# Performance work log

Measured on AMD Instinct MI355X. Metric: run time of the kernel, lower is better.

The kernel has to match this reference:

```python
import jax, jax.numpy as jnp
import numpy as np

N_NODES = 100000
N_EDGES = 1000000
DIM = 64
N_GRAPHS = 256
OUT_DIM = 10
BN_EPS = 1e-5


def setup_inputs() -> dict:
    key = jax.random.key(0)
    ks = jax.random.split(key, 12)
    s = 0.1  # weight init scale
    x = jax.random.normal(ks[0], (N_NODES, DIM), jnp.float32)
    edge_index = jax.random.randint(ks[1], (2, N_EDGES), 0, N_NODES, dtype=jnp.int32)
    batch = jnp.sort(jax.random.randint(ks[2], (N_NODES,), 0, N_GRAPHS, dtype=jnp.int32))
    w1 = jax.random.normal(ks[3], (3, DIM, DIM), jnp.float32) * s
    b1 = jax.random.normal(ks[4], (3, DIM), jnp.float32) * s
    w2 = jax.random.normal(ks[5], (3, DIM, DIM), jnp.float32) * s
    b2 = jax.random.normal(ks[6], (3, DIM), jnp.float32) * s
    gamma = jax.random.uniform(ks[7], (3, DIM), jnp.float32, 0.5, 1.5)
    beta = jax.random.normal(ks[8], (3, DIM), jnp.float32) * s
    eps_g = jnp.zeros((3,), jnp.float32)  # GIN train_eps, init 0
    lin_w = jax.random.normal(ks[9], (DIM, OUT_DIM), jnp.float32) * s
    lin_b = jax.random.normal(ks[10], (OUT_DIM,), jnp.float32) * s
    return dict(x=x, edge_index=edge_index, batch=batch, w1=w1, b1=b1,
                w2=w2, b2=b2, gamma=gamma, beta=beta, eps_g=eps_g,
                lin_w=lin_w, lin_b=lin_b)


def _gin_layer(x, src, dst, w1, b1, w2, b2, gamma, beta, eps):
    # scatter-add neighbor aggregation: agg[i] = sum_{(j->i) in E} x[j]
    agg = jax.ops.segment_sum(x[src], dst, num_segments=N_NODES)
    h = (1.0 + eps) * x + agg
    h = jax.nn.relu(h @ w1 + b1)
    h = jax.nn.relu(h @ w2 + b2)
    # BatchNorm1d, training-mode batch statistics (biased variance)
    mean = jnp.mean(h, axis=0)
    var = jnp.mean((h - mean) ** 2, axis=0)
    h = (h - mean) * jax.lax.rsqrt(var + BN_EPS) * gamma + beta
    return jax.nn.relu(h)  # outer F.relu(conv(...))


def reference(x, edge_index, batch, w1, b1, w2, b2, gamma, beta, eps_g, lin_w, lin_b):
    src, dst = edge_index[0], edge_index[1]
    for i in range(3):
        x = _gin_layer(x, src, dst, w1[i], b1[i], w2[i], b2[i],
                       gamma[i], beta[i], eps_g[i])
    # global mean pool over graphs
    sums = jax.ops.segment_sum(x, batch, num_segments=N_GRAPHS)
    counts = jax.ops.segment_sum(jnp.ones((x.shape[0],), x.dtype), batch,
                                 num_segments=N_GRAPHS)
    pooled = sums / jnp.maximum(counts, 1.0)[:, None]
    return pooled @ lin_w + lin_b
```

## Files before the change

kernel.cpp:

```cpp
#include <hip/hip_runtime.h>
#include <hip/hip_bf16.h>

#define N_NODES 100000
#define N_EDGES 1000000
#define DIM 64
#define N_GRAPHS 256
#define OUT_DIM 10
#define BN_EPS 1e-5f

#define POOL_BLOCKS 512
#define LAYER_BLOCKS ((N_NODES + 63) / 64)
#define PAD 24
#define SPILL_CAP 8192
#define NPART 8
#define PART_SZ ((N_NODES + NPART - 1) / NPART)

#define XC_BLOCKS ((N_NODES * 16 + 255) / 256)
#define NZERO_WORDS (384 + 16384 + 256 + N_NODES + 16)
#define NZERO4 (NZERO_WORDS / 4)
#define NZ_BLOCKS ((NZERO4 + 255) / 256)
#define PREP_BLOCKS (6 + XC_BLOCKS + NZ_BLOCKS + 1)

typedef __bf16 bf16x8 __attribute__((ext_vector_type(8)));
typedef float f32x4 __attribute__((ext_vector_type(4)));

__device__ __forceinline__ float bfu(unsigned short u) {
    return (float)__builtin_bit_cast(__bf16, u);
}

__global__ __launch_bounds__(256) void fill_kernel(
    const int* __restrict__ ei, int* __restrict__ deg,
    int* __restrict__ esrc, int* __restrict__ nspill, int* __restrict__ spill)
{
    const int part = blockIdx.x & (NPART - 1);
    const int e = (blockIdx.x >> 3) * 256 + threadIdx.x;
    if (e >= N_EDGES) return;
    int dst = ei[N_EDGES + e];
    int lo = part * PART_SZ;
    if (dst < lo || dst >= lo + PART_SZ) return;
    int src = ei[e];
    int pos = atomicAdd(&deg[dst], 1);
    if (pos < PAD) {
        esrc[dst * PAD + pos] = src;
    } else {
        int sp = atomicAdd(nspill, 1);
        if (sp < SPILL_CAP) { spill[2 * sp] = dst; spill[2 * sp + 1] = src; }
    }
}

__global__ __launch_bounds__(256) void prep_kernel(
    const float* __restrict__ w1, const float* __restrict__ w2,
    __bf16* __restrict__ wf,
    const float4* __restrict__ x0, ushort4* __restrict__ xp4,
    uint4* __restrict__ zbase,
    unsigned short* __restrict__ xp_s, unsigned short* __restrict__ xq_s,
    unsigned short* __restrict__ xs_s)
{
    const int bid = blockIdx.x;
    const int tid = threadIdx.x;
    if (bid < 6) {
        int L = bid >> 1, mat = bid & 1;
        const float* w = (mat ? w2 : w1) + L * 4096;
        __bf16* dst = wf + bid * 8192;
#pragma unroll
        for (int r = 0; r < 2; ++r) {
            int idx = tid + 256 * r;
            int lane = idx & 63;
            int kt = idx >> 6;
            int kstep = kt >> 2, nt = kt & 3;
            int n = nt * 16 + (lane & 15);
            int kbase = kstep * 32 + (lane >> 4) * 8;
#pragma unroll
            for (int j = 0; j < 8; ++j) {
                float v = w[(kbase + j) * 64 + n];
                __bf16 hi = (__bf16)v;
                dst[idx * 8 + j] = hi;
                dst[4096 + idx * 8 + j] = (__bf16)(v - (float)hi);
            }
        }
    } else if (bid < 6 + XC_BLOCKS) {
        int t = (bid - 6) * 256 + tid;
        if (t < N_NODES * 16) {
            float4 v = x0[t];
            ushort4 o;
            o.x = __builtin_bit_cast(unsigned short, (__bf16)v.x);
            o.y = __builtin_bit_cast(unsigned short, (__bf16)v.y);
            o.z = __builtin_bit_cast(unsigned short, (__bf16)v.z);
            o.w = __builtin_bit_cast(unsigned short, (__bf16)v.w);
            xp4[t] = o;
        }
    } else if (bid < 6 + XC_BLOCKS + NZ_BLOCKS) {
        int i = (bid - 6 - XC_BLOCKS) * 256 + tid;
        if (i < NZERO4) zbase[i] = (uint4){0u, 0u, 0u, 0u};
    } else {
        if (tid < 64) {
            xp_s[tid] = 0;
            xq_s[tid] = 0xFF80;
            xs_s[tid] = 0xFF80;
        }
    }
}

template <bool BN>
__global__ __launch_bounds__(256) void layer_kernel(
    const unsigned short* __restrict__ xb,
    const float* __restrict__ sums_in, const float* __restrict__ gamma,
    const float* __restrict__ beta,
    const int* __restrict__ deg, const int* __restrict__ esrc,
    const int* __restrict__ nspill, const int* __restrict__ spill,
    unsigned short* __restrict__ xbout,
    const __bf16* __restrict__ wf1, const __bf16* __restrict__ wf2,
    const float* __restrict__ b1, const float* __restrict__ b2,
    const float* __restrict__ eps_all, int layer,
    float* __restrict__ sums_out)
{
    __shared__ __attribute__((aligned(16))) unsigned tile[4][16][68];
    __shared__ float bnacc[128];

    const int tid = threadIdx.x;
    const int lane = tid & 63;
    const int wv = tid >> 6;
    const int q = lane >> 4;
    const int r = lane & 15;
    const int node0 = blockIdx.x * 64 + wv * 16;
    const bool active = node0 < N_NODES;

    if (tid < 128) bnacc[tid] = 0.0f;

    float scale = 1.0f, shift = 0.0f;
    if (BN) {
        const float inv_n = 1.0f / (float)N_NODES;
        float mean = sums_in[lane] * inv_n;
        float var = sums_in[64 + lane] * inv_n - mean * mean;
        scale = gamma[lane] * rsqrtf(var + BN_EPS);
        shift = fmaf(-mean, scale, beta[lane]);
    }

    f32x4 acc[4];
    float bs[4], bq[4];
#pragma unroll
    for (int nt = 0; nt < 4; ++nt) {
        acc[nt] = (f32x4){0.f, 0.f, 0.f, 0.f};
        bs[nt] = 0.0f; bq[nt] = 0.0f;
    }

    if (active) {
        const float epsv = 1.0f + eps_all[layer];

        int dvec = 0;
        if (lane < 16) dvec = deg[node0 + lane];
        uint4 nf0, nf1, nf2;
        {
            const uint4* ip = (const uint4*)(esrc + (size_t)node0 * PAD);
            nf0 = ip[0]; nf1 = ip[1]; nf2 = ip[2];
        }
        for (int i = 0; i < 16; ++i) {
            const uint4 c0 = nf0, c1 = nf1, c2 = nf2;
            if (i < 15) {
                const uint4* ip = (const uint4*)(esrc + (size_t)(node0 + i + 1) * PAD);
                nf0 = ip[0]; nf1 = ip[1]; nf2 = ip[2];
            }
            const int n = node0 + i;
            const int dfull = __builtin_amdgcn_readlane(dvec, i);
            const int d = min(dfull, PAD);

            float xv = bfu(xb[(size_t)n * 64 + lane]);
            if (BN) xv = fmaxf(fmaf(xv, scale, shift), 0.0f);
            float hval = epsv * xv;

            {
                unsigned idx[12] = {c0.x, c0.y, c0.z, c0.w, c1.x, c1.y,
                                    c1.z, c1.w, c2.x, c2.y, c2.z, c2.w};
                unsigned short u[12];
#pragma unroll
                for (int j = 0; j < 12; ++j) {
                    unsigned s = idx[j];
                    s = (s < (unsigned)N_NODES) ? s : (unsigned)N_NODES;
                    u[j] = xb[(size_t)s * 64 + lane];
                }
#pragma unroll
                for (int j = 0; j < 12; ++j) {
                    float t = bfu(u[j]);
                    if (BN) t = fmaxf(fmaf(t, scale, shift), 0.0f);
                    hval += t;
                }
            }
            if (d > 12) {
                const int* ep = esrc + (size_t)n * PAD + 12;
                unsigned short u[12];
#pragma unroll
                for (int j = 0; j < 12; ++j) {
                    unsigned s = (unsigned)ep[j];
                    s = (s < (unsigned)N_NODES) ? s : (unsigned)N_NODES;
                    u[j] = xb[(size_t)s * 64 + lane];
                }
#pragma unroll
                for (int j = 0; j < 12; ++j) {
                    float t = bfu(u[j]);
                    if (BN) t = fmaxf(fmaf(t, scale, shift), 0.0f);
                    hval += t;
                }
            }
            if (dfull > PAD) {
                int ns = min(*nspill, SPILL_CAP);
                for (int e = 0; e < ns; ++e) {
                    if (spill[2 * e] == n) {
                        float t = bfu(xb[(size_t)spill[2 * e + 1] * 64 + lane]);
                        if (BN) t = fmaxf(fmaf(t, scale, shift), 0.0f);
                        hval += t;
                    }
                }
            }
            __bf16 hi = (__bf16)hval;
            __bf16 lo = (__bf16)(hval - (float)hi);
            tile[wv][i][lane] = ((unsigned)__builtin_bit_cast(unsigned short, hi) << 16)
                              | (unsigned)__builtin_bit_cast(unsigned short, lo);
        }

        uint4 f0 = *(const uint4*)&tile[wv][r][q * 8];
        uint4 f1 = *(const uint4*)&tile[wv][r][q * 8 + 4];
        uint4 f2 = *(const uint4*)&tile[wv][r][32 + q * 8];
        uint4 f3 = *(const uint4*)&tile[wv][r][32 + q * 8 + 4];
#pragma unroll
        for (int kstep = 0; kstep < 2; ++kstep) {
            uint4 p0 = kstep ? f2 : f0;
            uint4 p1 = kstep ? f3 : f1;
            unsigned pk[8] = {p0.x, p0.y, p0.z, p0.w, p1.x, p1.y, p1.z, p1.w};
            bf16x8 ahi, alo;
#pragma unroll
            for (int j = 0; j < 8; ++j) {
                ahi[j] = __builtin_bit_cast(__bf16, (unsigned short)(pk[j] >> 16));
                alo[j] = __builtin_bit_cast(__bf16, (unsigned short)(pk[j] & 0xffffu));
            }
#pragma unroll
            for (int nt = 0; nt < 4; ++nt) {
                const __bf16* bp = wf1 + ((kstep * 4 + nt) * 64 + lane) * 8;
                bf16x8 bhi = *(const bf16x8*)bp;
                bf16x8 blo = *(const bf16x8*)(bp + 4096);
                acc[nt] = __builtin_amdgcn_mfma_f32_16x16x32_bf16(ahi, bhi, acc[nt], 0, 0, 0);
                acc[nt] = __builtin_amdgcn_mfma_f32_16x16x32_bf16(alo, bhi, acc[nt], 0, 0, 0);
                acc[nt] = __builtin_amdgcn_mfma_f32_16x16x32_bf16(ahi, blo, acc[nt], 0, 0, 0);
            }
        }
#pragma unroll
        for (int nt = 0; nt < 4; ++nt) {
            float b1v = b1[nt * 16 + r];
#pragma unroll
            for (int reg = 0; reg < 4; ++reg) {
                float v = fmaxf(acc[nt][reg] + b1v, 0.0f);
                __bf16 hi = (__bf16)v;
                __bf16 lo = (__bf16)(v - (float)hi);
                unsigned pk = ((unsigned)__builtin_bit_cast(unsigned short, hi) << 16)
                            | (unsigned)__builtin_bit_cast(unsigned short, lo);
                tile[wv][q * 4 + reg][nt * 16 + r] = pk;
            }
            acc[nt] = (f32x4){0.f, 0.f, 0.f, 0.f};
        }
#pragma unroll
        for (int kstep = 0; kstep < 2; ++kstep) {
            uint4 p0 = *(const uint4*)&tile[wv][r][kstep * 32 + q * 8];
            uint4 p1 = *(const uint4*)&tile[wv][r][kstep * 32 + q * 8 + 4];
            unsigned pk[8] = {p0.x, p0.y, p0.z, p0.w, p1.x, p1.y, p1.z, p1.w};
            bf16x8 ahi, alo;
#pragma unroll
            for (int j = 0; j < 8; ++j) {
                ahi[j] = __builtin_bit_cast(__bf16, (unsigned short)(pk[j] >> 16));
                alo[j] = __builtin_bit_cast(__bf16, (unsigned short)(pk[j] & 0xffffu));
            }
#pragma unroll
            for (int nt = 0; nt < 4; ++nt) {
                const __bf16* bp = wf2 + ((kstep * 4 + nt) * 64 + lane) * 8;
                bf16x8 bhi = *(const bf16x8*)bp;
                bf16x8 blo = *(const bf16x8*)(bp + 4096);
                acc[nt] = __builtin_amdgcn_mfma_f32_16x16x32_bf16(ahi, bhi, acc[nt], 0, 0, 0);
                acc[nt] = __builtin_amdgcn_mfma_f32_16x16x32_bf16(alo, bhi, acc[nt], 0, 0, 0);
                acc[nt] = __builtin_amdgcn_mfma_f32_16x16x32_bf16(ahi, blo, acc[nt], 0, 0, 0);
            }
        }
#pragma unroll
        for (int nt = 0; nt < 4; ++nt) {
            float b2v = b2[nt * 16 + r];
#pragma unroll
            for (int reg = 0; reg < 4; ++reg) {
                float v = fmaxf(acc[nt][reg] + b2v, 0.0f);
                size_t oi = (size_t)(node0 + q * 4 + reg) * 64 + nt * 16 + r;
                xbout[oi] = __builtin_bit_cast(unsigned short, (__bf16)v);
                bs[nt] += v;
                bq[nt] = fmaf(v, v, bq[nt]);
            }
        }
    }
    __syncthreads();
#pragma unroll
    for (int nt = 0; nt < 4; ++nt) {
        float s = bs[nt];
        s += __shfl_xor(s, 16);
        s += __shfl_xor(s, 32);
        float ss = bq[nt];
        ss += __shfl_xor(ss, 16);
        ss += __shfl_xor(ss, 32);
        if (q == 0) {
            atomicAdd(&bnacc[nt * 16 + r], s);
            atomicAdd(&bnacc[64 + nt * 16 + r], ss);
        }
    }
    __syncthreads();
    if (tid < 128) unsafeAtomicAdd(&sums_out[tid], bnacc[tid]);
}

__global__ __launch_bounds__(256) void pool_kernel(
    const unsigned short* __restrict__ h2b, const float* __restrict__ sums,
    const float* __restrict__ gamma, const float* __restrict__ beta,
    const int* __restrict__ batch,
    float* __restrict__ pooled, float* __restrict__ counts)
{
    const int lane = threadIdx.x & 63;
    const int w = blockIdx.x * 4 + (threadIdx.x >> 6);
    const int nw = POOL_BLOCKS * 4;
    const int npw = (N_NODES + nw - 1) / nw;
    int n0 = w * npw;
    if (n0 >= N_NODES) return;
    int n1 = n0 + npw;
    if (n1 > N_NODES) n1 = N_NODES;

    const float inv_n = 1.0f / (float)N_NODES;
    float mean = sums[lane] * inv_n;
    float var = sums[64 + lane] * inv_n - mean * mean;
    const float scale = gamma[lane] * rsqrtf(var + BN_EPS);
    const float shift = fmaf(-mean, scale, beta[lane]);

    int cur = batch[n0];
    float acc = 0.0f, cnt = 0.0f;
    for (int n = n0; n < n1; ++n) {
        int g = batch[n];
        if (g != cur) {
            unsafeAtomicAdd(&pooled[cur * 64 + lane], acc);
            if (lane == 0) unsafeAtomicAdd(&counts[cur], cnt);
            acc = 0.0f; cnt = 0.0f; cur = g;
        }
        float v = bfu(h2b[(size_t)n * 64 + lane]);
        v = fmaxf(fmaf(v, scale, shift), 0.0f);
        acc += v;
        cnt += 1.0f;
    }
    unsafeAtomicAdd(&pooled[cur * 64 + lane], acc);
    if (lane == 0) unsafeAtomicAdd(&counts[cur], cnt);
}

__global__ __launch_bounds__(256) void final_kernel(
    const float* __restrict__ pooled, const float* __restrict__ counts,
    const float* __restrict__ lin_w, const float* __restrict__ lin_b,
    float* __restrict__ out)
{
    int t = blockIdx.x * 256 + threadIdx.x;
    if (t >= N_GRAPHS * OUT_DIM) return;
    int g = t / OUT_DIM;
    int o = t - g * OUT_DIM;
    float acc = 0.0f;
#pragma unroll 8
    for (int d = 0; d < 64; ++d)
        acc = fmaf(pooled[g * 64 + d], lin_w[d * OUT_DIM + o], acc);
    float c = fmaxf(counts[g], 1.0f);
    out[t] = acc / c + lin_b[o];
}

extern "C" void kernel_launch(void* const* d_in, const int* in_sizes, int n_in,
                              void* d_out, int out_size, void* d_ws, size_t ws_size,
                              hipStream_t stream)
{
    const float* x0    = (const float*)d_in[0];
    const int*   ei    = (const int*)d_in[1];
    const int*   batch = (const int*)d_in[2];
    const float* w1    = (const float*)d_in[3];
    const float* b1    = (const float*)d_in[4];
    const float* w2    = (const float*)d_in[5];
    const float* b2    = (const float*)d_in[6];
    const float* gamma = (const float*)d_in[7];
    const float* beta  = (const float*)d_in[8];
    const float* eps_g = (const float*)d_in[9];
    const float* lin_w = (const float*)d_in[10];
    const float* lin_b = (const float*)d_in[11];
    float* out = (float*)d_out;

    float* ws   = (float*)d_ws;
    float* SUMS = ws;
    float* POOL = SUMS + 384;
    float* CNT  = POOL + N_GRAPHS * 64;
    int*   DEG    = (int*)(CNT + N_GRAPHS);
    int*   NSPILL = DEG + N_NODES;
    __bf16* WF  = (__bf16*)(NSPILL + 16);
    int*   SPILL  = (int*)(WF + 6 * 8192);
    int*   ESRC   = SPILL + 2 * SPILL_CAP;
    unsigned short* XP = (unsigned short*)(ESRC + (size_t)N_NODES * PAD);
    unsigned short* XQ = XP + (size_t)(N_NODES + 1) * 64;
    unsigned short* XS = XQ + (size_t)(N_NODES + 1) * 64;
    unsigned short* XR = XS + (size_t)(N_NODES + 1) * 64;

    const int fill_blocks = ((N_EDGES + 255) / 256) * NPART;

    prep_kernel<<<PREP_BLOCKS, 256, 0, stream>>>(
        w1, w2, WF, (const float4*)x0, (ushort4*)XP, (uint4*)SUMS,
        XP + (size_t)N_NODES * 64, XQ + (size_t)N_NODES * 64,
        XS + (size_t)N_NODES * 64);
    fill_kernel<<<fill_blocks, 256, 0, stream>>>(ei, DEG, ESRC, NSPILL, SPILL);

    layer_kernel<false><<<LAYER_BLOCKS, 256, 0, stream>>>(
        XP, nullptr, nullptr, nullptr, DEG, ESRC, NSPILL, SPILL, XQ,
        WF, WF + 8192, b1, b2, eps_g, 0, SUMS);

    layer_kernel<true><<<LAYER_BLOCKS, 256, 0, stream>>>(
        XQ, SUMS, gamma, beta, DEG, ESRC, NSPILL, SPILL, XS,
        WF + 16384, WF + 24576, b1 + 64, b2 + 64, eps_g, 1, SUMS + 128);

    layer_kernel<true><<<LAYER_BLOCKS, 256, 0, stream>>>(
        XS, SUMS + 128, gamma + 64, beta + 64, DEG, ESRC, NSPILL, SPILL, XR,
        WF + 32768, WF + 40960, b1 + 128, b2 + 128, eps_g, 2, SUMS + 256);

    pool_kernel<<<POOL_BLOCKS, 256, 0, stream>>>(
        XR, SUMS + 256, gamma + 128, beta + 128, batch, POOL, CNT);
    final_kernel<<<(N_GRAPHS * OUT_DIM + 255) / 256, 256, 0, stream>>>(
        POOL, CNT, lin_w, lin_b, out);
}
```

Baseline: 372.6 us.

## Merge prep and fill kernels, fuse final linear into pool via last-block pattern

Fill and prep work now run as one kernel distinguished by block index, with degree/spill counters zeroed by a memset beforehand instead of inside prep. The final linear layer moves into the pool kernel, where the last block to finish (found with an atomic counter and threadfences) computes the output. This removes two kernel launches and their inter-kernel gaps. In exchange it adds a memset call, and the final projection runs on a single block.

```diff
diff --git a/kernel.cpp b/kernel.cpp
--- a/kernel.cpp
+++ b/kernel.cpp
@@ -15,11 +15,12 @@
 #define NPART 8
 #define PART_SZ ((N_NODES + NPART - 1) / NPART)
 
+#define FILL_BLOCKS (((N_EDGES + 255) / 256) * NPART)
 #define XC_BLOCKS ((N_NODES * 16 + 255) / 256)
-#define NZERO_WORDS (384 + 16384 + 256 + N_NODES + 16)
+#define NZERO_WORDS (384 + 16384 + 256)
 #define NZERO4 (NZERO_WORDS / 4)
 #define NZ_BLOCKS ((NZERO4 + 255) / 256)
-#define PREP_BLOCKS (6 + XC_BLOCKS + NZ_BLOCKS + 1)
+#define PREPFILL_BLOCKS (FILL_BLOCKS + 6 + XC_BLOCKS + NZ_BLOCKS + 1)
 
 typedef __bf16 bf16x8 __attribute__((ext_vector_type(8)));
 typedef float f32x4 __attribute__((ext_vector_type(4)));
@@ -28,27 +29,9 @@
     return (float)__builtin_bit_cast(__bf16, u);
 }
 
-__global__ __launch_bounds__(256) void fill_kernel(
+__global__ __launch_bounds__(256) void prepfill_kernel(
     const int* __restrict__ ei, int* __restrict__ deg,
-    int* __restrict__ esrc, int* __restrict__ nspill, int* __restrict__ spill)
-{
-    const int part = blockIdx.x & (NPART - 1);
-    const int e = (blockIdx.x >> 3) * 256 + threadIdx.x;
-    if (e >= N_EDGES) return;
-    int dst = ei[N_EDGES + e];
-    int lo = part * PART_SZ;
-    if (dst < lo || dst >= lo + PART_SZ) return;
-    int src = ei[e];
-    int pos = atomicAdd(&deg[dst], 1);
-    if (pos < PAD) {
-        esrc[dst * PAD + pos] = src;
-    } else {
-        int sp = atomicAdd(nspill, 1);
-        if (sp < SPILL_CAP) { spill[2 * sp] = dst; spill[2 * sp + 1] = src; }
-    }
-}
-
-__global__ __launch_bounds__(256) void prep_kernel(
+    int* __restrict__ esrc, int* __restrict__ nspill, int* __restrict__ spill,
     const float* __restrict__ w1, const float* __restrict__ w2,
     __bf16* __restrict__ wf,
     const float4* __restrict__ x0, ushort4* __restrict__ xp4,
@@ -58,10 +41,28 @@
 {
     const int bid = blockIdx.x;
     const int tid = threadIdx.x;
-    if (bid < 6) {
-        int L = bid >> 1, mat = bid & 1;
+    if (bid < FILL_BLOCKS) {
+        const int part = bid & (NPART - 1);
+        const int e = (bid >> 3) * 256 + tid;
+        if (e >= N_EDGES) return;
+        int dst = ei[N_EDGES + e];
+        int lo = part * PART_SZ;
+        if (dst < lo || dst >= lo + PART_SZ) return;
+        int src = ei[e];
+        int pos = atomicAdd(&deg[dst], 1);
+        if (pos < PAD) {
+            esrc[dst * PAD + pos] = src;
+        } else {
+            int sp = atomicAdd(nspill, 1);
+            if (sp < SPILL_CAP) { spill[2 * sp] = dst; spill[2 * sp + 1] = src; }
+        }
+        return;
+    }
+    const int b = bid - FILL_BLOCKS;
+    if (b < 6) {
+        int L = b >> 1, mat = b & 1;
         const float* w = (mat ? w2 : w1) + L * 4096;
-        __bf16* dst = wf + bid * 8192;
+        __bf16* dst = wf + b * 8192;
 #pragma unroll
         for (int r = 0; r < 2; ++r) {
             int idx = tid + 256 * r;
@@ -78,8 +79,8 @@
                 dst[4096 + idx * 8 + j] = (__bf16)(v - (float)hi);
             }
         }
-    } else if (bid < 6 + XC_BLOCKS) {
-        int t = (bid - 6) * 256 + tid;
+    } else if (b < 6 + XC_BLOCKS) {
+        int t = (b - 6) * 256 + tid;
         if (t < N_NODES * 16) {
             float4 v = x0[t];
             ushort4 o;
@@ -89,8 +90,8 @@
             o.w = __builtin_bit_cast(unsigned short, (__bf16)v.w);
             xp4[t] = o;
         }
-    } else if (bid < 6 + XC_BLOCKS + NZ_BLOCKS) {
-        int i = (bid - 6 - XC_BLOCKS) * 256 + tid;
+    } else if (b < 6 + XC_BLOCKS + NZ_BLOCKS) {
+        int i = (b - 6 - XC_BLOCKS) * 256 + tid;
         if (i < NZERO4) zbase[i] = (uint4){0u, 0u, 0u, 0u};
     } else {
         if (tid < 64) {
@@ -312,56 +313,62 @@
     const unsigned short* __restrict__ h2b, const float* __restrict__ sums,
     const float* __restrict__ gamma, const float* __restrict__ beta,
     const int* __restrict__ batch,
-    float* __restrict__ pooled, float* __restrict__ counts)
+    const float* __restrict__ lin_w, const float* __restrict__ lin_b,
+    float* __restrict__ pooled, float* __restrict__ counts,
+    int* __restrict__ pfcnt, float* __restrict__ out)
 {
     const int lane = threadIdx.x & 63;
     const int w = blockIdx.x * 4 + (threadIdx.x >> 6);
     const int nw = POOL_BLOCKS * 4;
     const int npw = (N_NODES + nw - 1) / nw;
     int n0 = w * npw;
-    if (n0 >= N_NODES) return;
-    int n1 = n0 + npw;
-    if (n1 > N_NODES) n1 = N_NODES;
-
-    const float inv_n = 1.0f / (float)N_NODES;
-    float mean = sums[lane] * inv_n;
-    float var = sums[64 + lane] * inv_n - mean * mean;
-    const float scale = gamma[lane] * rsqrtf(var + BN_EPS);
-    const float shift = fmaf(-mean, scale, beta[lane]);
-
-    int cur = batch[n0];
-    float acc = 0.0f, cnt = 0.0f;
-    for (int n = n0; n < n1; ++n) {
-        int g = batch[n];
-        if (g != cur) {
-            unsafeAtomicAdd(&pooled[cur * 64 + lane], acc);
-            if (lane == 0) unsafeAtomicAdd(&counts[cur], cnt);
-            acc = 0.0f; cnt = 0.0f; cur = g;
-        }
-        float v = bfu(h2b[(size_t)n * 64 + lane]);
-        v = fmaxf(fmaf(v, scale, shift), 0.0f);
-        acc += v;
-        cnt += 1.0f;
-    }
-    unsafeAtomicAdd(&pooled[cur * 64 + lane], acc);
-    if (lane == 0) unsafeAtomicAdd(&counts[cur], cnt);
-}
-
-__global__ __launch_bounds__(256) void final_kernel(
-    const float* __restrict__ pooled, const float* __restrict__ counts,
-    const float* __restrict__ lin_w, const float* __restrict__ lin_b,
-    float* __restrict__ out)
-{
-    int t = blockIdx.x * 256 + threadIdx.x;
-    if (t >= N_GRAPHS * OUT_DIM) return;
-    int g = t / OUT_DIM;
-    int o = t - g * OUT_DIM;
-    float acc = 0.0f;
+
+    if (n0 < N_NODES) {
+        int n1 = min(n0 + npw, N_NODES);
+        const float inv_n = 1.0f / (float)N_NODES;
+        float mean = sums[lane] * inv_n;
+        float var = sums[64 + lane] * inv_n - mean * mean;
+        const float scale = gamma[lane] * rsqrtf(var + BN_EPS);
+        const float shift = fmaf(-mean, scale, beta[lane]);
+
+        int cur = batch[n0];
+        float acc = 0.0f, cnt = 0.0f;
+        for (int n = n0; n < n1; ++n) {
+            int g = batch[n];
+            if (g != cur) {
+                unsafeAtomicAdd(&pooled[cur * 64 + lane], acc);
+                if (lane == 0) unsafeAtomicAdd(&counts[cur], cnt);
+                acc = 0.0f; cnt = 0.0f; cur = g;
+            }
+            float v = bfu(h2b[(size_t)n * 64 + lane]);
+            v = fmaxf(fmaf(v, scale, shift), 0.0f);
+            acc += v;
+            cnt += 1.0f;
+        }
+        unsafeAtomicAdd(&pooled[cur * 64 + lane], acc);
+        if (lane == 0) unsafeAtomicAdd(&counts[cur], cnt);
+    }
+
+    __syncthreads();
+    __shared__ int amlast;
+    if (threadIdx.x == 0) {
+        __threadfence();
+        amlast = (atomicAdd(pfcnt, 1) == POOL_BLOCKS - 1) ? 1 : 0;
+    }
+    __syncthreads();
+    if (amlast) {
+        __threadfence();
+        for (int t = threadIdx.x; t < N_GRAPHS * OUT_DIM; t += 256) {
+            int g = t / OUT_DIM;
+            int o = t - g * OUT_DIM;
+            float acc = 0.0f;
 #pragma unroll 8
-    for (int d = 0; d < 64; ++d)
-        acc = fmaf(pooled[g * 64 + d], lin_w[d * OUT_DIM + o], acc);
-    float c = fmaxf(counts[g], 1.0f);
-    out[t] = acc / c + lin_b[o];
+            for (int d = 0; d < 64; ++d)
+                acc = fmaf(pooled[g * 64 + d], lin_w[d * OUT_DIM + o], acc);
+            float c = fmaxf(counts[g], 1.0f);
+            out[t] = acc / c + lin_b[o];
+        }
+    }
 }
 
 extern "C" void kernel_launch(void* const* d_in, const int* in_sizes, int n_in,
@@ -388,7 +395,8 @@
     float* CNT  = POOL + N_GRAPHS * 64;
     int*   DEG    = (int*)(CNT + N_GRAPHS);
     int*   NSPILL = DEG + N_NODES;
-    __bf16* WF  = (__bf16*)(NSPILL + 16);
+    int*   PFCNT  = NSPILL + 16;
+    __bf16* WF  = (__bf16*)(PFCNT + 16);
     int*   SPILL  = (int*)(WF + 6 * 8192);
     int*   ESRC   = SPILL + 2 * SPILL_CAP;
     unsigned short* XP = (unsigned short*)(ESRC + (size_t)N_NODES * PAD);
@@ -396,13 +404,12 @@
     unsigned short* XS = XQ + (size_t)(N_NODES + 1) * 64;
     unsigned short* XR = XS + (size_t)(N_NODES + 1) * 64;
 
-    const int fill_blocks = ((N_EDGES + 255) / 256) * NPART;
-
-    prep_kernel<<<PREP_BLOCKS, 256, 0, stream>>>(
+    hipMemsetAsync(DEG, 0, (N_NODES + 32) * sizeof(int), stream);
+    prepfill_kernel<<<PREPFILL_BLOCKS, 256, 0, stream>>>(
+        ei, DEG, ESRC, NSPILL, SPILL,
         w1, w2, WF, (const float4*)x0, (ushort4*)XP, (uint4*)SUMS,
         XP + (size_t)N_NODES * 64, XQ + (size_t)N_NODES * 64,
         XS + (size_t)N_NODES * 64);
-    fill_kernel<<<fill_blocks, 256, 0, stream>>>(ei, DEG, ESRC, NSPILL, SPILL);
 
     layer_kernel<false><<<LAYER_BLOCKS, 256, 0, stream>>>(
         XP, nullptr, nullptr, nullptr, DEG, ESRC, NSPILL, SPILL, XQ,
@@ -417,7 +424,6 @@
         WF + 32768, WF + 40960, b1 + 128, b2 + 128, eps_g, 2, SUMS + 256);
 
     pool_kernel<<<POOL_BLOCKS, 256, 0, stream>>>(
-        XR, SUMS + 256, gamma + 128, beta + 128, batch, POOL, CNT);
-    final_kernel<<<(N_GRAPHS * OUT_DIM + 255) / 256, 256, 0, stream>>>(
-        POOL, CNT, lin_w, lin_b, out);
+        XR, SUMS + 256, gamma + 128, beta + 128, batch, lin_w, lin_b,
+        POOL, CNT, PFCNT, out);
 }
```

Measured after the change: 385.5 us. +3.5%, slower.
